# Kernel tuning notes

Hardware: AMD Instinct MI355X
Metric: run time of the kernel (lower is better)

## Reference

```python
import jax, jax.numpy as jnp
import numpy as np

B_SZ, SEQ, H, P = 4, 8192, 512, 256


def _s5(x, lam_re, lam_im, log_dt, b_re, b_im, c_re, c_im, d):
    """Single-direction S5 diagonal SSM. x: [B,L,H] -> y: [B,L,H]."""
    lam = lam_re + 1j * lam_im                      # [P] complex diagonal A
    dt = jnp.exp(log_dt)                            # [P] ZOH timestep
    a_bar = jnp.exp(lam * dt)                       # [P] discretized A
    b_bar = ((a_bar - 1.0) / lam)[:, None] * (b_re + 1j * b_im)  # [P,H]
    bu = jnp.einsum('blh,ph->blp', x.astype(b_bar.dtype), b_bar)  # [B,L,P]
    a_el = jnp.broadcast_to(a_bar, bu.shape)        # time-invariant A per step

    def comb(e1, e2):  # associative combine for linear recurrence
        a1, s1 = e1
        a2, s2 = e2
        return (a1 * a2, a2 * s1 + s2)

    _, states = jax.lax.associative_scan(comb, (a_el, bu), axis=1)  # [B,L,P]
    c = c_re + 1j * c_im                            # [H,P]
    return jnp.einsum('blp,hp->blh', states, c).real + x * d


def setup_inputs() -> dict:
    key = jax.random.key(0)
    ks = jax.random.split(key, 10)
    return {
        'x': jax.random.normal(ks[0], (B_SZ, SEQ, H), dtype=jnp.float32),
        'Lambda_re': -0.1 - 0.5 * jax.random.uniform(ks[1], (2, P), dtype=jnp.float32),
        'Lambda_im': jnp.pi * jax.random.normal(ks[2], (2, P), dtype=jnp.float32),
        'log_dt': jnp.log(0.001) + (jnp.log(0.1) - jnp.log(0.001)) * jax.random.uniform(ks[3], (2, P), dtype=jnp.float32),
        'B_re': jax.random.normal(ks[4], (2, P, H), dtype=jnp.float32) / np.sqrt(H),
        'B_im': jax.random.normal(ks[5], (2, P, H), dtype=jnp.float32) / np.sqrt(H),
        'C_re': jax.random.normal(ks[6], (2, H, P), dtype=jnp.float32) / np.sqrt(P),
        'C_im': jax.random.normal(ks[7], (2, H, P), dtype=jnp.float32) / np.sqrt(P),
        'D': jax.random.normal(ks[8], (2, H), dtype=jnp.float32),
    }


def reference(x, Lambda_re, Lambda_im, log_dt, B_re, B_im, C_re, C_im, D):
    # fwd(x) + flip(bwd(flip(x)))
    y_f = _s5(x, Lambda_re[0], Lambda_im[0], log_dt[0], B_re[0], B_im[0], C_re[0], C_im[0], D[0])
    x_r = x[:, ::-1]
    y_b = _s5(x_r, Lambda_re[1], Lambda_im[1], log_dt[1], B_re[1], B_im[1], C_re[1], C_im[1], D[1])[:, ::-1]
    return y_f + y_b
```

## Files before the change

### kernel.cpp

```cpp
#include <hip/hip_runtime.h>
#include <math.h>

typedef unsigned short ushort_t;
typedef __bf16 bf16x8 __attribute__((ext_vector_type(8)));
typedef ushort_t ushort8v __attribute__((ext_vector_type(8)));
typedef float f32x4 __attribute__((ext_vector_type(4)));

#define B_SZ   4
#define SEQ    8192
#define M_ROWS (B_SZ * SEQ)
#define CH     128
#define NC     (SEQ / CH)

__device__ __forceinline__ ushort_t f2bf(float f) {
    unsigned u = __float_as_uint(f);
    u = u + 0x7fffu + ((u >> 16) & 1u);
    return (ushort_t)(u >> 16);
}
__device__ __forceinline__ float bf2f(ushort_t b) {
    return __uint_as_float(((unsigned)b) << 16);
}

__device__ __forceinline__ void load16_lds(const void* g, void* l) {
    __builtin_amdgcn_global_load_lds(
        (const __attribute__((address_space(1))) unsigned int*)g,
        (__attribute__((address_space(3))) unsigned int*)l, 16, 0, 0);
}

__device__ __forceinline__ bf16x8 ldfrag(const ushort_t* p) {
    union { ushort8v u; bf16x8 b; } cv;
    cv.u = *(const ushort8v*)p;
    return cv.b;
}

__global__ void prep_kernel(const float* __restrict__ Lre,
                            const float* __restrict__ Lim,
                            const float* __restrict__ ldt,
                            const float* __restrict__ Bre,
                            const float* __restrict__ Bim,
                            const float* __restrict__ Cre,
                            const float* __restrict__ Cim,
                            float* __restrict__ abar,
                            float* __restrict__ apow,
                            ushort_t* __restrict__ Bmat,
                            ushort_t* __restrict__ Cmat) {
    int idx = blockIdx.x * 256 + threadIdx.x;
    int h = idx & 511;
    int p = (idx >> 9) & 255;
    int d = idx >> 17;
    int ip = d * 256 + p;
    float lr = Lre[ip], li = Lim[ip];
    float dt = expf(ldt[ip]);
    float e   = expf(lr * dt);
    float ang = li * dt;
    float ar = e * cosf(ang), ai = e * sinf(ang);
    float nr = ar - 1.0f, ni = ai;
    float den = lr * lr + li * li;
    float cr = (nr * lr + ni * li) / den;
    float ci = (ni * lr - nr * li) / den;
    float br = Bre[idx], bi = Bim[idx];
    Bmat[(d * 512 + 2 * p) * 512 + h]     = f2bf(cr * br - ci * bi);
    Bmat[(d * 512 + 2 * p + 1) * 512 + h] = f2bf(cr * bi + ci * br);
    if (h == 0) {
        int o = d * 512 + 2 * p;
        abar[o] = ar;  abar[o + 1] = ai;
        float eC = expf(lr * dt * (float)CH);
        float aC = ang * (float)CH;
        apow[o] = eC * cosf(aC);  apow[o + 1] = eC * sinf(aC);
    }
    int p2 = idx & 255;
    int h2 = (idx >> 8) & 511;
    int d2 = idx >> 17;
    Cmat[h2 * 1024 + d2 * 512 + 2 * p2]     = f2bf(Cre[idx]);
    Cmat[h2 * 1024 + d2 * 512 + 2 * p2 + 1] = f2bf(-Cim[idx]);
}

__global__ void conv_x_kernel(const float* __restrict__ x,
                              ushort_t* __restrict__ X16) {
    int i = blockIdx.x * 256 + threadIdx.x;
    float4 v = ((const float4*)x)[i];
    ushort_t o[4] = {f2bf(v.x), f2bf(v.y), f2bf(v.z), f2bf(v.w)};
    *(uint2*)&X16[(size_t)i * 4] = *(const uint2*)o;
}

template<int EPI, int KD_, int NT>
__global__ __launch_bounds__(512, 2)
void gemm_8ph(const ushort_t* __restrict__ A, const ushort_t* __restrict__ Bm,
              ushort_t* __restrict__ Cb, float* __restrict__ Cf,
              const float* __restrict__ X, const float* __restrict__ Dv) {
    __shared__ ushort_t shA[2][2][256 * 32];
    __shared__ ushort_t shB[2][2][256 * 32];
    constexpr int NKT = KD_ / 64;

    const int tid  = threadIdx.x;
    const int lane = tid & 63;
    const int wv   = tid >> 6;
    const int wr = wv >> 2, wc = wv & 3;
    const int l15 = lane & 15, lq = lane >> 4;

    const int lin = blockIdx.x;
    const int xcd = lin & 7;
    const int j   = lin >> 3;
    const int mt  = xcd * 16 + j / NT;
    const int nt  = j % NT;
    const int m0 = mt * 256;
    const int n0 = nt * 256;
    const int CN = NT * 256;

    f32x4 acc[8][4];
#pragma unroll
    for (int i = 0; i < 8; ++i)
#pragma unroll
        for (int jj = 0; jj < 4; ++jj)
            acc[i][jj] = (f32x4){0.f, 0.f, 0.f, 0.f};

    const int srow = wv * 32 + (lane >> 2);
    const int sck  = (((lane & 3) ^ ((lane >> 3) & 3))) * 8;
    const ushort_t* Ag = A  + (size_t)(m0 + srow) * KD_ + sck;
    const ushort_t* Bg = Bm + (size_t)(n0 + srow) * KD_ + sck;

#define STAGE_A(t, ks) do {                                                   \
        const ushort_t* g_ = Ag + (size_t)(t) * 64 + (ks) * 32;               \
        ushort_t* d_ = &shA[(t) & 1][(ks)][wv * 1024];                        \
        load16_lds(g_, d_);                                                   \
        load16_lds(g_ + (size_t)16 * KD_, d_ + 512);                          \
    } while (0)
#define STAGE_B(t, ks) do {                                                   \
        const ushort_t* g_ = Bg + (size_t)(t) * 64 + (ks) * 32;               \
        ushort_t* d_ = &shB[(t) & 1][(ks)][wv * 1024];                        \
        load16_lds(g_, d_);                                                   \
        load16_lds(g_ + (size_t)16 * KD_, d_ + 512);                          \
    } while (0)

    const int rdoff = ((lq ^ ((l15 >> 1) & 3))) * 8;
    const int rdA = (wr * 128 + l15) * 32 + rdoff;
    const int rdB = (wc * 64  + l15) * 32 + rdoff;

#define MFMA_PH(bx, by, nlo) do {                                             \
        __builtin_amdgcn_s_setprio(1);                                        \
        _Pragma("unroll")                                                     \
        for (int mi_ = 0; mi_ < 8; ++mi_) {                                   \
            acc[mi_][nlo]     = __builtin_amdgcn_mfma_f32_16x16x32_bf16(      \
                af[mi_], bx, acc[mi_][nlo], 0, 0, 0);                         \
            acc[mi_][nlo + 1] = __builtin_amdgcn_mfma_f32_16x16x32_bf16(      \
                af[mi_], by, acc[mi_][nlo + 1], 0, 0, 0);                     \
        }                                                                     \
        __builtin_amdgcn_s_setprio(0);                                        \
    } while (0)

    STAGE_A(0, 0); STAGE_A(0, 1); STAGE_B(0, 0); STAGE_B(0, 1);
    STAGE_A(1, 0); STAGE_B(1, 0); STAGE_A(1, 1);
    asm volatile("s_waitcnt vmcnt(6)" ::: "memory");
    __builtin_amdgcn_s_barrier();

    bf16x8 af[8];
#pragma unroll 2
    for (int kt = 0; kt < NKT; ++kt) {
        const int buf = kt & 1;
        const ushort_t* aS0 = &shA[buf][0][rdA];
        const ushort_t* aS1 = &shA[buf][1][rdA];
        const ushort_t* bS0 = &shB[buf][0][rdB];
        const ushort_t* bS1 = &shB[buf][1][rdB];

        {
#pragma unroll
            for (int mi = 0; mi < 8; ++mi) af[mi] = ldfrag(aS0 + mi * 512);
            bf16x8 b0 = ldfrag(bS0), b1 = ldfrag(bS0 + 512);
            if (kt + 1 < NKT) STAGE_B(kt + 1, 1);
            __builtin_amdgcn_s_barrier();
            MFMA_PH(b0, b1, 0);
            __builtin_amdgcn_s_barrier();
        }
        {
            bf16x8 b2 = ldfrag(bS0 + 1024), b3 = ldfrag(bS0 + 1536);
            if (kt + 2 < NKT) STAGE_A(kt + 2, 0);
            __builtin_amdgcn_s_barrier();
            MFMA_PH(b2, b3, 2);
            __builtin_amdgcn_s_barrier();
        }
        {
#pragma unroll
            for (int mi = 0; mi < 8; ++mi) af[mi] = ldfrag(aS1 + mi * 512);
            bf16x8 b0 = ldfrag(bS1), b1 = ldfrag(bS1 + 512);
            if (kt + 2 < NKT) STAGE_B(kt + 2, 0);
            __builtin_amdgcn_s_barrier();
            MFMA_PH(b0, b1, 0);
            __builtin_amdgcn_s_barrier();
        }
        {
            bf16x8 b2 = ldfrag(bS1 + 1024), b3 = ldfrag(bS1 + 1536);
            if (kt + 2 < NKT) STAGE_A(kt + 2, 1);
            __builtin_amdgcn_s_barrier();
            MFMA_PH(b2, b3, 2);
            if (kt + 1 < NKT) {
                if (kt + 2 < NKT)
                    asm volatile("s_waitcnt vmcnt(6)" ::: "memory");
                else
                    asm volatile("s_waitcnt vmcnt(0)" ::: "memory");
                __builtin_amdgcn_s_barrier();
            }
        }
    }
#undef STAGE_A
#undef STAGE_B
#undef MFMA_PH

#pragma unroll
    for (int mi = 0; mi < 8; ++mi) {
#pragma unroll
        for (int ni = 0; ni < 4; ++ni) {
            const int col = n0 + wc * 64 + ni * 16 + l15;
            float dsum = 0.f;
            if (EPI == 1) dsum = Dv[col] + Dv[512 + col];
#pragma unroll
            for (int r = 0; r < 4; ++r) {
                const int row = m0 + wr * 128 + mi * 16 + lq * 4 + r;
                if (EPI == 0) {
                    Cb[(size_t)row * CN + col] = f2bf(acc[mi][ni][r]);
                } else {
                    const size_t idx = (size_t)row * 512 + col;
                    Cf[idx] = acc[mi][ni][r] + X[idx] * dsum;
                }
            }
        }
    }
}

__global__ __launch_bounds__(512)
void scan_carry(const ushort_t* __restrict__ S, const float* __restrict__ abar,
                float* __restrict__ carry) {
    int b = blockIdx.x, c = blockIdx.y, t = threadIdx.x;
    int dir = t >> 8, p = t & 255;
    float ar = abar[dir * 512 + 2 * p], ai = abar[dir * 512 + 2 * p + 1];
    float sr = 0.f, si = 0.f;
    const ushort_t* base = S + ((size_t)b * SEQ + (size_t)c * CH) * 1024
                             + dir * 512 + 2 * p;
    for (int ii = 0; ii < CH; ++ii) {
        int i = dir ? (CH - 1 - ii) : ii;
        unsigned u = *(const unsigned*)(base + (size_t)i * 1024);
        float re = bf2f((ushort_t)(u & 0xffffu));
        float im = bf2f((ushort_t)(u >> 16));
        float nr = fmaf(ar, sr, fmaf(-ai, si, re));
        float ni = fmaf(ar, si, fmaf(ai, sr, im));
        sr = nr; si = ni;
    }
    int o = (b * NC + c) * 1024 + dir * 512 + 2 * p;
    carry[o] = sr; carry[o + 1] = si;
}

__global__ __launch_bounds__(512)
void scan_comb(const float* __restrict__ carry, float* __restrict__ init,
               const float* __restrict__ apow) {
    int b = blockIdx.x, t = threadIdx.x;
    int dir = t >> 8, p = t & 255;
    float pr = apow[dir * 512 + 2 * p], pi = apow[dir * 512 + 2 * p + 1];
    float sr = 0.f, si = 0.f;
    for (int cc = 0; cc < NC; ++cc) {
        int c = dir ? (NC - 1 - cc) : cc;
        int o = (b * NC + c) * 1024 + dir * 512 + 2 * p;
        init[o] = sr; init[o + 1] = si;
        float cr = carry[o], ci = carry[o + 1];
        float nr = fmaf(pr, sr, fmaf(-pi, si, cr));
        float ni = fmaf(pr, si, fmaf(pi, sr, ci));
        sr = nr; si = ni;
    }
}

__global__ __launch_bounds__(512)
void scan_final(ushort_t* __restrict__ S, const float* __restrict__ abar,
                const float* __restrict__ init) {
    int b = blockIdx.x, c = blockIdx.y, t = threadIdx.x;
    int dir = t >> 8, p = t & 255;
    float ar = abar[dir * 512 + 2 * p], ai = abar[dir * 512 + 2 * p + 1];
    int o = (b * NC + c) * 1024 + dir * 512 + 2 * p;
    float sr = init[o], si = init[o + 1];
    ushort_t* base = S + ((size_t)b * SEQ + (size_t)c * CH) * 1024
                       + dir * 512 + 2 * p;
    for (int ii = 0; ii < CH; ++ii) {
        int i = dir ? (CH - 1 - ii) : ii;
        unsigned* addr = (unsigned*)(base + (size_t)i * 1024);
        unsigned u = *addr;
        float re = bf2f((ushort_t)(u & 0xffffu));
        float im = bf2f((ushort_t)(u >> 16));
        float nr = fmaf(ar, sr, fmaf(-ai, si, re));
        float ni = fmaf(ar, si, fmaf(ai, sr, im));
        sr = nr; si = ni;
        *addr = ((unsigned)f2bf(si) << 16) | (unsigned)f2bf(sr);
    }
}

extern "C" void kernel_launch(void* const* d_in, const int* in_sizes, int n_in,
                              void* d_out, int out_size, void* d_ws, size_t ws_size,
                              hipStream_t stream) {
    const float* x   = (const float*)d_in[0];
    const float* Lre = (const float*)d_in[1];
    const float* Lim = (const float*)d_in[2];
    const float* ldt = (const float*)d_in[3];
    const float* Bre = (const float*)d_in[4];
    const float* Bim = (const float*)d_in[5];
    const float* Cre = (const float*)d_in[6];
    const float* Cim = (const float*)d_in[7];
    const float* Dv  = (const float*)d_in[8];
    float* y = (float*)d_out;
    char* ws = (char*)d_ws;

    ushort_t* SB16 = (ushort_t*)(ws);
    ushort_t* X16  = (ushort_t*)(ws + 67108864);
    ushort_t* Bm16 = (ushort_t*)(ws + 100663296);
    ushort_t* Cm16 = (ushort_t*)(ws + 101711872);
    float* abar  = (float*)(ws + 102760448);
    float* apow  = (float*)(ws + 102764544);
    float* carry = (float*)(ws + 67108864);
    float* initb = (float*)(ws + 68157440);

    prep_kernel<<<1024, 256, 0, stream>>>(Lre, Lim, ldt, Bre, Bim, Cre, Cim,
                                          abar, apow, Bm16, Cm16);
    conv_x_kernel<<<16384, 256, 0, stream>>>(x, X16);

    gemm_8ph<0, 512, 4><<<512, 512, 0, stream>>>(X16, Bm16, SB16, nullptr,
                                                 nullptr, nullptr);

    dim3 gs(B_SZ, NC);
    scan_carry<<<gs, 512, 0, stream>>>(SB16, abar, carry);
    scan_comb<<<B_SZ, 512, 0, stream>>>(carry, initb, apow);
    scan_final<<<gs, 512, 0, stream>>>(SB16, abar, initb);

    gemm_8ph<1, 1024, 2><<<256, 512, 0, stream>>>(SB16, Cm16, nullptr, y,
                                                  x, Dv);
}
```

Measured before the change: 268.6 us.

## Pair M-tiles per block in first GEMM and fold carry combine into final scan

The first GEMM now launches half as many blocks, and each block processes two consecutive 256-row M tiles through one continuous load/MFMA pipeline. The first tile's epilogue is written mid-loop, so the prefetch for the second tile overlaps it. Separately, the serial scan_comb kernel is removed: each scan_fin2 block recomputes its own chunk-initial state by walking the preceding carries. This removes one launch and its serial bottleneck but adds redundant O(NC) work per block. Pairing tiles halves the grid (256 blocks), which may underfill the CUs.

```diff
diff --git a/kernel.cpp b/kernel.cpp
--- a/kernel.cpp
+++ b/kernel.cpp
@@ -83,14 +83,16 @@
     *(uint2*)&X16[(size_t)i * 4] = *(const uint2*)o;
 }
 
-template<int EPI, int KD_, int NT>
+template<int EPI, int KD_, int NT, int NPAIR>
 __global__ __launch_bounds__(512, 2)
 void gemm_8ph(const ushort_t* __restrict__ A, const ushort_t* __restrict__ Bm,
               ushort_t* __restrict__ Cb, float* __restrict__ Cf,
               const float* __restrict__ X, const float* __restrict__ Dv) {
     __shared__ ushort_t shA[2][2][256 * 32];
     __shared__ ushort_t shB[2][2][256 * 32];
-    constexpr int NKT = KD_ / 64;
+    constexpr int NKT    = KD_ / 64;
+    constexpr int TT     = NKT * NPAIR;
+    constexpr int LOGNKT = (KD_ == 512) ? 3 : 4;
 
     const int tid  = threadIdx.x;
     const int lane = tid & 63;
@@ -101,9 +103,9 @@
     const int lin = blockIdx.x;
     const int xcd = lin & 7;
     const int j   = lin >> 3;
-    const int mt  = xcd * 16 + j / NT;
+    const int mp  = xcd * (16 / NPAIR) + j / NT;
     const int nt  = j % NT;
-    const int m0 = mt * 256;
+    const int m0 = mp * 256 * NPAIR;
     const int n0 = nt * 256;
     const int CN = NT * 256;
 
@@ -120,13 +122,15 @@
     const ushort_t* Bg = Bm + (size_t)(n0 + srow) * KD_ + sck;
 
 #define STAGE_A(t, ks) do {                                                   \
-        const ushort_t* g_ = Ag + (size_t)(t) * 64 + (ks) * 32;               \
+        const ushort_t* g_ = Ag                                               \
+            + (NPAIR > 1 ? (size_t)((t) >> LOGNKT) * (256u * KD_) : 0)        \
+            + (size_t)((t) & (NKT - 1)) * 64 + (ks) * 32;                     \
         ushort_t* d_ = &shA[(t) & 1][(ks)][wv * 1024];                        \
         load16_lds(g_, d_);                                                   \
         load16_lds(g_ + (size_t)16 * KD_, d_ + 512);                          \
     } while (0)
 #define STAGE_B(t, ks) do {                                                   \
-        const ushort_t* g_ = Bg + (size_t)(t) * 64 + (ks) * 32;               \
+        const ushort_t* g_ = Bg + (size_t)((t) & (NKT - 1)) * 64 + (ks) * 32; \
         ushort_t* d_ = &shB[(t) & 1][(ks)][wv * 1024];                        \
         load16_lds(g_, d_);                                                   \
         load16_lds(g_ + (size_t)16 * KD_, d_ + 512);                          \
@@ -148,6 +152,29 @@
         __builtin_amdgcn_s_setprio(0);                                        \
     } while (0)
 
+#define EPILOGUE(TB) do {                                                     \
+        _Pragma("unroll")                                                     \
+        for (int mi = 0; mi < 8; ++mi) {                                      \
+            _Pragma("unroll")                                                 \
+            for (int ni = 0; ni < 4; ++ni) {                                  \
+                const int col = n0 + wc * 64 + ni * 16 + l15;                 \
+                float dsum = 0.f;                                             \
+                if (EPI == 1) dsum = Dv[col] + Dv[512 + col];                 \
+                _Pragma("unroll")                                             \
+                for (int r = 0; r < 4; ++r) {                                 \
+                    const int row = m0 + (TB) * 256 + wr * 128 + mi * 16      \
+                                    + lq * 4 + r;                             \
+                    if (EPI == 0) {                                           \
+                        Cb[(size_t)row * CN + col] = f2bf(acc[mi][ni][r]);    \
+                    } else {                                                  \
+                        const size_t idx = (size_t)row * 512 + col;           \
+                        Cf[idx] = acc[mi][ni][r] + X[idx] * dsum;             \
+                    }                                                         \
+                }                                                             \
+            }                                                                 \
+        }                                                                     \
+    } while (0)
+
     STAGE_A(0, 0); STAGE_A(0, 1); STAGE_B(0, 0); STAGE_B(0, 1);
     STAGE_A(1, 0); STAGE_B(1, 0); STAGE_A(1, 1);
     asm volatile("s_waitcnt vmcnt(6)" ::: "memory");
@@ -155,7 +182,7 @@
 
     bf16x8 af[8];
 #pragma unroll 2
-    for (int kt = 0; kt < NKT; ++kt) {
+    for (int kt = 0; kt < TT; ++kt) {
         const int buf = kt & 1;
         const ushort_t* aS0 = &shA[buf][0][rdA];
         const ushort_t* aS1 = &shA[buf][1][rdA];
@@ -166,14 +193,14 @@
 #pragma unroll
             for (int mi = 0; mi < 8; ++mi) af[mi] = ldfrag(aS0 + mi * 512);
             bf16x8 b0 = ldfrag(bS0), b1 = ldfrag(bS0 + 512);
-            if (kt + 1 < NKT) STAGE_B(kt + 1, 1);
+            if (kt + 1 < TT) STAGE_B(kt + 1, 1);
             __builtin_amdgcn_s_barrier();
             MFMA_PH(b0, b1, 0);
             __builtin_amdgcn_s_barrier();
         }
         {
             bf16x8 b2 = ldfrag(bS0 + 1024), b3 = ldfrag(bS0 + 1536);
-            if (kt + 2 < NKT) STAGE_A(kt + 2, 0);
+            if (kt + 2 < TT) STAGE_A(kt + 2, 0);
             __builtin_amdgcn_s_barrier();
             MFMA_PH(b2, b3, 2);
             __builtin_amdgcn_s_barrier();
@@ -182,48 +209,39 @@
 #pragma unroll
             for (int mi = 0; mi < 8; ++mi) af[mi] = ldfrag(aS1 + mi * 512);
             bf16x8 b0 = ldfrag(bS1), b1 = ldfrag(bS1 + 512);
-            if (kt + 2 < NKT) STAGE_B(kt + 2, 0);
+            if (kt + 2 < TT) STAGE_B(kt + 2, 0);
             __builtin_amdgcn_s_barrier();
             MFMA_PH(b0, b1, 0);
             __builtin_amdgcn_s_barrier();
         }
         {
             bf16x8 b2 = ldfrag(bS1 + 1024), b3 = ldfrag(bS1 + 1536);
-            if (kt + 2 < NKT) STAGE_A(kt + 2, 1);
+            if (kt + 2 < TT) STAGE_A(kt + 2, 1);
             __builtin_amdgcn_s_barrier();
             MFMA_PH(b2, b3, 2);
-            if (kt + 1 < NKT) {
-                if (kt + 2 < NKT)
+            if (kt + 1 < TT) {
+                if (kt + 2 < TT)
                     asm volatile("s_waitcnt vmcnt(6)" ::: "memory");
                 else
                     asm volatile("s_waitcnt vmcnt(0)" ::: "memory");
                 __builtin_amdgcn_s_barrier();
             }
         }
+        if (NPAIR == 2 && kt == NKT - 1) {
+            EPILOGUE(0);
+#pragma unroll
+            for (int i2 = 0; i2 < 8; ++i2)
+#pragma unroll
+                for (int j2 = 0; j2 < 4; ++j2)
+                    acc[i2][j2] = (f32x4){0.f, 0.f, 0.f, 0.f};
+        }
     }
 #undef STAGE_A
 #undef STAGE_B
 #undef MFMA_PH
 
-#pragma unroll
-    for (int mi = 0; mi < 8; ++mi) {
-#pragma unroll
-        for (int ni = 0; ni < 4; ++ni) {
-            const int col = n0 + wc * 64 + ni * 16 + l15;
-            float dsum = 0.f;
-            if (EPI == 1) dsum = Dv[col] + Dv[512 + col];
-#pragma unroll
-            for (int r = 0; r < 4; ++r) {
-                const int row = m0 + wr * 128 + mi * 16 + lq * 4 + r;
-                if (EPI == 0) {
-                    Cb[(size_t)row * CN + col] = f2bf(acc[mi][ni][r]);
-                } else {
-                    const size_t idx = (size_t)row * 512 + col;
-                    Cf[idx] = acc[mi][ni][r] + X[idx] * dsum;
-                }
-            }
-        }
-    }
+    EPILOGUE(NPAIR - 1);
+#undef EPILOGUE
 }
 
 __global__ __launch_bounds__(512)
@@ -249,31 +267,30 @@
 }
 
 __global__ __launch_bounds__(512)
-void scan_comb(const float* __restrict__ carry, float* __restrict__ init,
-               const float* __restrict__ apow) {
-    int b = blockIdx.x, t = threadIdx.x;
-    int dir = t >> 8, p = t & 255;
-    float pr = apow[dir * 512 + 2 * p], pi = apow[dir * 512 + 2 * p + 1];
-    float sr = 0.f, si = 0.f;
-    for (int cc = 0; cc < NC; ++cc) {
-        int c = dir ? (NC - 1 - cc) : cc;
-        int o = (b * NC + c) * 1024 + dir * 512 + 2 * p;
-        init[o] = sr; init[o + 1] = si;
-        float cr = carry[o], ci = carry[o + 1];
-        float nr = fmaf(pr, sr, fmaf(-pi, si, cr));
-        float ni = fmaf(pr, si, fmaf(pi, sr, ci));
-        sr = nr; si = ni;
-    }
-}
-
-__global__ __launch_bounds__(512)
-void scan_final(ushort_t* __restrict__ S, const float* __restrict__ abar,
-                const float* __restrict__ init) {
+void scan_fin2(ushort_t* __restrict__ S, const float* __restrict__ abar,
+               const float* __restrict__ apow, const float* __restrict__ carry) {
     int b = blockIdx.x, c = blockIdx.y, t = threadIdx.x;
     int dir = t >> 8, p = t & 255;
     float ar = abar[dir * 512 + 2 * p], ai = abar[dir * 512 + 2 * p + 1];
-    int o = (b * NC + c) * 1024 + dir * 512 + 2 * p;
-    float sr = init[o], si = init[o + 1];
+    float pr = apow[dir * 512 + 2 * p], pi = apow[dir * 512 + 2 * p + 1];
+    float sr = 0.f, si = 0.f;
+    if (dir == 0) {
+        for (int cc = 0; cc < c; ++cc) {
+            int o = (b * NC + cc) * 1024 + 2 * p;
+            float cr0 = carry[o], ci0 = carry[o + 1];
+            float nr = fmaf(pr, sr, fmaf(-pi, si, cr0));
+            float ni = fmaf(pr, si, fmaf(pi, sr, ci0));
+            sr = nr; si = ni;
+        }
+    } else {
+        for (int cc = NC - 1; cc > c; --cc) {
+            int o = (b * NC + cc) * 1024 + 512 + 2 * p;
+            float cr0 = carry[o], ci0 = carry[o + 1];
+            float nr = fmaf(pr, sr, fmaf(-pi, si, cr0));
+            float ni = fmaf(pr, si, fmaf(pi, sr, ci0));
+            sr = nr; si = ni;
+        }
+    }
     ushort_t* base = S + ((size_t)b * SEQ + (size_t)c * CH) * 1024
                        + dir * 512 + 2 * p;
     for (int ii = 0; ii < CH; ++ii) {
@@ -311,20 +328,18 @@
     float* abar  = (float*)(ws + 102760448);
     float* apow  = (float*)(ws + 102764544);
     float* carry = (float*)(ws + 67108864);
-    float* initb = (float*)(ws + 68157440);
 
     prep_kernel<<<1024, 256, 0, stream>>>(Lre, Lim, ldt, Bre, Bim, Cre, Cim,
                                           abar, apow, Bm16, Cm16);
     conv_x_kernel<<<16384, 256, 0, stream>>>(x, X16);
 
-    gemm_8ph<0, 512, 4><<<512, 512, 0, stream>>>(X16, Bm16, SB16, nullptr,
-                                                 nullptr, nullptr);
+    gemm_8ph<0, 512, 4, 2><<<256, 512, 0, stream>>>(X16, Bm16, SB16, nullptr,
+                                                    nullptr, nullptr);
 
     dim3 gs(B_SZ, NC);
     scan_carry<<<gs, 512, 0, stream>>>(SB16, abar, carry);
-    scan_comb<<<B_SZ, 512, 0, stream>>>(carry, initb, apow);
-    scan_final<<<gs, 512, 0, stream>>>(SB16, abar, initb);
-
-    gemm_8ph<1, 1024, 2><<<256, 512, 0, stream>>>(SB16, Cm16, nullptr, y,
-                                                  x, Dv);
-}
+    scan_fin2<<<gs, 512, 0, stream>>>(SB16, abar, apow, carry);
+
+    gemm_8ph<1, 1024, 2, 1><<<256, 512, 0, stream>>>(SB16, Cm16, nullptr, y,
+                                                     x, Dv);
+}
```

New measurement: 275.1 us. +2.4%, slower.

## Fuse chunk carry computation into B-projection GEMM epilogue and merge scan kernels

Applied to the files above, without the earlier changes.

The first GEMM's epilogue now computes each 128-row chunk's local scan carry directly from the bf16-rounded accumulators, using precomputed powers of a_bar and cross-lane shuffles. This removes the scan_carry pass, which reread the whole state tensor. The separate scan_comb kernel is also dropped: each scan_fin2 block recomputes its own chunk prefix from the carries. That adds redundant serial work per block, up to 63 steps, but saves one launch and one full memory pass. Carry and power buffers are placed in the output buffer as scratch before the final GEMM overwrites it.

```diff
diff --git a/kernel.cpp b/kernel.cpp
--- a/kernel.cpp
+++ b/kernel.cpp
@@ -31,6 +31,10 @@
     union { ushort8v u; bf16x8 b; } cv;
     cv.u = *(const ushort8v*)p;
     return cv.b;
+}
+
+__device__ __forceinline__ float2 cmul(float2 a, float2 b) {
+    return make_float2(a.x * b.x - a.y * b.y, a.x * b.y + a.y * b.x);
 }
 
 __global__ void prep_kernel(const float* __restrict__ Lre,
@@ -42,6 +46,7 @@
                             const float* __restrict__ Cim,
                             float* __restrict__ abar,
                             float* __restrict__ apow,
+                            float* __restrict__ PW,
                             ushort_t* __restrict__ Bmat,
                             ushort_t* __restrict__ Cmat) {
     int idx = blockIdx.x * 256 + threadIdx.x;
@@ -67,6 +72,15 @@
         float eC = expf(lr * dt * (float)CH);
         float aC = ang * (float)CH;
         apow[o] = eC * cosf(aC);  apow[o + 1] = eC * sinf(aC);
+        float2 a1 = make_float2(ar, ai);
+        float2 a2 = cmul(a1, a1);
+        float2 a4 = cmul(a2, a2);
+        float2 a8 = cmul(a4, a4);
+        float2 a16 = cmul(a8, a8);
+        int q = d * 256 + p;
+        PW[q * 6 + 0] = a1.x;  PW[q * 6 + 1] = a1.y;
+        PW[q * 6 + 2] = a4.x;  PW[q * 6 + 3] = a4.y;
+        PW[q * 6 + 4] = a16.x; PW[q * 6 + 5] = a16.y;
     }
     int p2 = idx & 255;
     int h2 = (idx >> 8) & 511;
@@ -87,7 +101,8 @@
 __global__ __launch_bounds__(512, 2)
 void gemm_8ph(const ushort_t* __restrict__ A, const ushort_t* __restrict__ Bm,
               ushort_t* __restrict__ Cb, float* __restrict__ Cf,
-              const float* __restrict__ X, const float* __restrict__ Dv) {
+              const float* __restrict__ X, const float* __restrict__ Dv,
+              const float* __restrict__ PW, float* __restrict__ CAR) {
     __shared__ ushort_t shA[2][2][256 * 32];
     __shared__ ushort_t shB[2][2][256 * 32];
     constexpr int NKT = KD_ / 64;
@@ -224,56 +239,92 @@
             }
         }
     }
+
+    if (EPI == 0) {
+        const int dirq = n0 >> 9;
+        const bool evn = ((l15 & 1) == 0);
+        const int cidx = ((m0 >> 7) + wr) * 1024;
+
+#define CACC(MI, R, CC) do {                                                  \
+            float vo = bf2f(f2bf(acc[MI][ni][R]));                            \
+            float vp = __shfl_xor(vo, 1);                                     \
+            float vr = evn ? vo : vp;                                         \
+            float vi = evn ? vp : vo;                                         \
+            wr_ = fmaf(CC.x, vr, fmaf(-CC.y, vi, wr_));                       \
+            wi_ = fmaf(CC.x, vi, fmaf(CC.y, vr, wi_));                        \
+        } while (0)
+#define CSTEP(MI) do {                                                        \
+            float wr_ = 0.f, wi_ = 0.f;                                       \
+            CACC(MI, 0, c0); CACC(MI, 1, c1);                                 \
+            CACC(MI, 2, c2); CACC(MI, 3, c3);                                 \
+            float comp = evn ? (t16.x * wr_ - t16.y * wi_)                    \
+                             : (t16.x * wi_ + t16.y * wr_);                   \
+            csum += comp;                                                     \
+            t16 = cmul(t16, A16);                                             \
+        } while (0)
+
+#pragma unroll
+        for (int ni = 0; ni < 4; ++ni) {
+            const int col = n0 + wc * 64 + ni * 16 + l15;
+            const int q = col >> 1;
+            float2 A1  = make_float2(PW[q * 6 + 0], PW[q * 6 + 1]);
+            float2 A4  = make_float2(PW[q * 6 + 2], PW[q * 6 + 3]);
+            float2 A16 = make_float2(PW[q * 6 + 4], PW[q * 6 + 5]);
+            const int lqp = dirq ? lq : 3 - lq;
+            float2 A4_2 = cmul(A4, A4);
+            float2 A4_3 = cmul(A4_2, A4);
+            float2 P4 = (lqp == 0) ? make_float2(1.f, 0.f)
+                       : (lqp == 1) ? A4
+                       : (lqp == 2) ? A4_2 : A4_3;
+            float2 c0, c1, c2, c3;
+            if (dirq == 0) {
+                c3 = P4; c2 = cmul(c3, A1); c1 = cmul(c2, A1); c0 = cmul(c1, A1);
+            } else {
+                c0 = P4; c1 = cmul(c0, A1); c2 = cmul(c1, A1); c3 = cmul(c2, A1);
+            }
+            float2 t16 = make_float2(1.f, 0.f);
+            float csum = 0.f;
+            if (dirq == 0) {
+                CSTEP(7); CSTEP(6); CSTEP(5); CSTEP(4);
+                CSTEP(3); CSTEP(2); CSTEP(1); CSTEP(0);
+            } else {
+                CSTEP(0); CSTEP(1); CSTEP(2); CSTEP(3);
+                CSTEP(4); CSTEP(5); CSTEP(6); CSTEP(7);
+            }
+            csum += __shfl_xor(csum, 16);
+            csum += __shfl_xor(csum, 32);
+            if (lq == 0) CAR[cidx + col] = csum;
+        }
+#undef CACC
+#undef CSTEP
+    }
 }
 
 __global__ __launch_bounds__(512)
-void scan_carry(const ushort_t* __restrict__ S, const float* __restrict__ abar,
-                float* __restrict__ carry) {
+void scan_fin2(ushort_t* __restrict__ S, const float* __restrict__ abar,
+               const float* __restrict__ apow, const float* __restrict__ carry) {
     int b = blockIdx.x, c = blockIdx.y, t = threadIdx.x;
     int dir = t >> 8, p = t & 255;
     float ar = abar[dir * 512 + 2 * p], ai = abar[dir * 512 + 2 * p + 1];
-    float sr = 0.f, si = 0.f;
-    const ushort_t* base = S + ((size_t)b * SEQ + (size_t)c * CH) * 1024
-                             + dir * 512 + 2 * p;
-    for (int ii = 0; ii < CH; ++ii) {
-        int i = dir ? (CH - 1 - ii) : ii;
-        unsigned u = *(const unsigned*)(base + (size_t)i * 1024);
-        float re = bf2f((ushort_t)(u & 0xffffu));
-        float im = bf2f((ushort_t)(u >> 16));
-        float nr = fmaf(ar, sr, fmaf(-ai, si, re));
-        float ni = fmaf(ar, si, fmaf(ai, sr, im));
-        sr = nr; si = ni;
-    }
-    int o = (b * NC + c) * 1024 + dir * 512 + 2 * p;
-    carry[o] = sr; carry[o + 1] = si;
-}
-
-__global__ __launch_bounds__(512)
-void scan_comb(const float* __restrict__ carry, float* __restrict__ init,
-               const float* __restrict__ apow) {
-    int b = blockIdx.x, t = threadIdx.x;
-    int dir = t >> 8, p = t & 255;
     float pr = apow[dir * 512 + 2 * p], pi = apow[dir * 512 + 2 * p + 1];
     float sr = 0.f, si = 0.f;
-    for (int cc = 0; cc < NC; ++cc) {
-        int c = dir ? (NC - 1 - cc) : cc;
-        int o = (b * NC + c) * 1024 + dir * 512 + 2 * p;
-        init[o] = sr; init[o + 1] = si;
-        float cr = carry[o], ci = carry[o + 1];
-        float nr = fmaf(pr, sr, fmaf(-pi, si, cr));
-        float ni = fmaf(pr, si, fmaf(pi, sr, ci));
-        sr = nr; si = ni;
-    }
-}
-
-__global__ __launch_bounds__(512)
-void scan_final(ushort_t* __restrict__ S, const float* __restrict__ abar,
-                const float* __restrict__ init) {
-    int b = blockIdx.x, c = blockIdx.y, t = threadIdx.x;
-    int dir = t >> 8, p = t & 255;
-    float ar = abar[dir * 512 + 2 * p], ai = abar[dir * 512 + 2 * p + 1];
-    int o = (b * NC + c) * 1024 + dir * 512 + 2 * p;
-    float sr = init[o], si = init[o + 1];
+    if (dir == 0) {
+        for (int cc = 0; cc < c; ++cc) {
+            int o = (b * NC + cc) * 1024 + 2 * p;
+            float cr0 = carry[o], ci0 = carry[o + 1];
+            float nr = fmaf(pr, sr, fmaf(-pi, si, cr0));
+            float ni = fmaf(pr, si, fmaf(pi, sr, ci0));
+            sr = nr; si = ni;
+        }
+    } else {
+        for (int cc = NC - 1; cc > c; --cc) {
+            int o = (b * NC + cc) * 1024 + 512 + 2 * p;
+            float cr0 = carry[o], ci0 = carry[o + 1];
+            float nr = fmaf(pr, sr, fmaf(-pi, si, cr0));
+            float ni = fmaf(pr, si, fmaf(pi, sr, ci0));
+            sr = nr; si = ni;
+        }
+    }
     ushort_t* base = S + ((size_t)b * SEQ + (size_t)c * CH) * 1024
                        + dir * 512 + 2 * p;
     for (int ii = 0; ii < CH; ++ii) {
@@ -310,21 +361,19 @@
     ushort_t* Cm16 = (ushort_t*)(ws + 101711872);
     float* abar  = (float*)(ws + 102760448);
     float* apow  = (float*)(ws + 102764544);
-    float* carry = (float*)(ws + 67108864);
-    float* initb = (float*)(ws + 68157440);
+    float* carry = (float*)d_out;
+    float* PW    = (float*)((char*)d_out + 1048576);
 
     prep_kernel<<<1024, 256, 0, stream>>>(Lre, Lim, ldt, Bre, Bim, Cre, Cim,
-                                          abar, apow, Bm16, Cm16);
+                                          abar, apow, PW, Bm16, Cm16);
     conv_x_kernel<<<16384, 256, 0, stream>>>(x, X16);
 
     gemm_8ph<0, 512, 4><<<512, 512, 0, stream>>>(X16, Bm16, SB16, nullptr,
-                                                 nullptr, nullptr);
+                                                 nullptr, nullptr, PW, carry);
 
     dim3 gs(B_SZ, NC);
-    scan_carry<<<gs, 512, 0, stream>>>(SB16, abar, carry);
-    scan_comb<<<B_SZ, 512, 0, stream>>>(carry, initb, apow);
-    scan_final<<<gs, 512, 0, stream>>>(SB16, abar, initb);
+    scan_fin2<<<gs, 512, 0, stream>>>(SB16, abar, apow, carry);
 
     gemm_8ph<1, 1024, 2><<<256, 512, 0, stream>>>(SB16, Cm16, nullptr, y,
-                                                  x, Dv);
-}
+                                                  x, Dv, nullptr, nullptr);
+}
```

New measurement: 271.7 us. Within noise of the previous version (+1.2%).
